# Performance work log

Measured on AMD Instinct MI355X. Metric: run time of the kernel, lower is better.

## Reference

```python
import jax, jax.numpy as jnp
import numpy as np

B, T, C, HEAD = 8, 2048, 1024, 64

def setup_inputs() -> dict:
    key = jax.random.key(0)
    kx, kq, kk, kv = jax.random.split(key, 4)
    bound = 1.0 / np.sqrt(C)  # torch Linear default init range
    x = jax.random.normal(kx, (B, T, C), dtype=jnp.float32)
    Wq = jax.random.uniform(kq, (C, HEAD), jnp.float32, -bound, bound)
    Wk = jax.random.uniform(kk, (C, HEAD), jnp.float32, -bound, bound)
    Wv = jax.random.uniform(kv, (C, HEAD), jnp.float32, -bound, bound)
    return {"x": x, "Wq": Wq, "Wk": Wk, "Wv": Wv}

def reference(x, Wq, Wk, Wv):
    Bn, Tn, Cn = x.shape
    q = jnp.einsum('btc,ch->bth', x, Wq)  # [B,T,H]
    k = jnp.einsum('btc,ch->bth', x, Wk)
    v = jnp.einsum('btc,ch->bth', x, Wv)
    # NOTE: original scales by C**-0.5 (input channels), not head_size**-0.5
    scale = Cn ** (-0.5)
    w = jnp.einsum('bqh,bkh->bqk', q, k) * scale  # [B,T,T]
    causal = jnp.tril(jnp.ones((Tn, Tn), dtype=bool))
    w = jnp.where(causal, w, -jnp.inf)
    wei = jax.nn.softmax(w, axis=-1)
    return jnp.einsum('bqk,bkh->bqh', wei, v)  # [B,T,H]
```

## Files before the change

kernel.cpp:

```cpp
#include <hip/hip_runtime.h>
#include <hip/hip_bf16.h>

#define B_ 8
#define T_ 2048
#define C_ 1024
#define H_ 64

typedef __bf16 bf16x8 __attribute__((ext_vector_type(8)));
typedef float f32x4 __attribute__((ext_vector_type(4)));

typedef __attribute__((address_space(3))) unsigned int lds_u32;
typedef const __attribute__((address_space(1))) unsigned int glb_u32;
__device__ __forceinline__ void gl_lds16(const void* gp, void* lp) {
  __builtin_amdgcn_global_load_lds((glb_u32*)gp, (lds_u32*)lp, 16, 0, 0);
}

__global__ __launch_bounds__(256) void prep_w_k(const float* __restrict__ Wq,
                                                const float* __restrict__ Wk,
                                                const float* __restrict__ Wv,
                                                __bf16* __restrict__ Wt2) {
  int idx = blockIdx.x * 256 + threadIdx.x;
  int m = idx >> 14;
  int rem = idx & 16383;
  int h = rem >> 8;
  int cb = (rem & 255) * 4;
  const float* W = (m == 0) ? Wq : ((m == 1) ? Wk : Wv);
  float sc = (m == 0) ? 0.03125f : 1.0f;
  const int col = m * 64 + h;
  const int t = cb >> 5;
  const int g = (cb >> 3) & 3;
  const int j = cb & 7;
  __bf16* dst = Wt2 + (((size_t)(t * 4 + g) * 192 + col) * 8 + j);
#pragma unroll
  for (int i = 0; i < 4; ++i) dst[i] = (__bf16)(W[(size_t)(cb + i) * H_ + h] * sc);
}

__global__ __launch_bounds__(256) void qkv_k(const float* __restrict__ x,
                                             const __bf16* __restrict__ Wt2,
                                             __bf16* __restrict__ q,
                                             __bf16* __restrict__ kk,
                                             __bf16* __restrict__ vt) {
  __shared__ __align__(16) char smem[65536];
  const int tid = threadIdx.x;
  const int lane = tid & 63;
  const int wc = tid >> 6;
  const int l15 = lane & 15;
  const int g = lane >> 4;
  const int row0 = blockIdx.x * 32;

  const int srow = tid >> 3;
  const int sch = (tid & 7) ^ (srow & 7);
  const char* agsrc = (const char*)(x + (size_t)(row0 + srow) * C_) + sch * 16;
  const int adst = tid * 16;
  const char* b2src = (const char*)Wt2 + tid * 16;

  f32x4 acc[2][3];
#pragma unroll
  for (int rt = 0; rt < 2; ++rt)
#pragma unroll
    for (int ctl = 0; ctl < 3; ++ctl) acc[rt][ctl] = (f32x4)0.0f;

  auto stage = [&](int t, int bufo) {
    gl_lds16(agsrc + ((size_t)t << 7), smem + bufo + adst);
    const char* bs = b2src + (size_t)t * 12288;
    gl_lds16(bs, smem + bufo + 4096 + tid * 16);
    gl_lds16(bs + 4096, smem + bufo + 8192 + tid * 16);
    gl_lds16(bs + 8192, smem + bufo + 12288 + tid * 16);
  };

  stage(0, 0);
  stage(1, 16384);
  stage(2, 32768);

  for (int t = 0; t < 32; ++t) {
    const int rem = 31 - t;
    if (rem >= 2) {
      asm volatile("s_waitcnt vmcnt(8)" ::: "memory");
    } else if (rem == 1) {
      asm volatile("s_waitcnt vmcnt(4)" ::: "memory");
    } else {
      asm volatile("s_waitcnt vmcnt(0)" ::: "memory");
    }
    __builtin_amdgcn_s_barrier();
    if (t + 3 < 32) stage(t + 3, ((t + 3) & 3) << 14);
    const int cur = (t & 3) << 14;
    bf16x8 af[2];
#pragma unroll
    for (int rt = 0; rt < 2; ++rt) {
      const int row = rt * 16 + l15;
      const char* ab = smem + cur + row * 128;
      f32x4 a0 = *(const f32x4*)(ab + ((((g << 1)) ^ (row & 7)) << 4));
      f32x4 a1 = *(const f32x4*)(ab + ((((g << 1) | 1) ^ (row & 7)) << 4));
#pragma unroll
      for (int j = 0; j < 4; ++j) {
        af[rt][j] = (__bf16)a0[j];
        af[rt][4 + j] = (__bf16)a1[j];
      }
    }
#pragma unroll
    for (int ctl = 0; ctl < 3; ++ctl) {
      const int col = wc * 48 + ctl * 16 + l15;
      bf16x8 bf = *(const bf16x8*)(smem + cur + 4096 + g * 3072 + col * 16);
      acc[0][ctl] = __builtin_amdgcn_mfma_f32_16x16x32_bf16(af[0], bf, acc[0][ctl], 0, 0, 0);
      acc[1][ctl] = __builtin_amdgcn_mfma_f32_16x16x32_bf16(af[1], bf, acc[1][ctl], 0, 0, 0);
    }
  }

#pragma unroll
  for (int rt = 0; rt < 2; ++rt)
#pragma unroll
    for (int ctl = 0; ctl < 3; ++ctl) {
      const int cb = wc * 48 + ctl * 16;
      const int m = cb >> 6;
      const int drow = row0 + rt * 16 + g * 4;
      if (m == 0) {
#pragma unroll
        for (int r = 0; r < 4; ++r)
          q[(size_t)(drow + r) * H_ + (cb & 63) + l15] = (__bf16)acc[rt][ctl][r];
      } else if (m == 1) {
#pragma unroll
        for (int r = 0; r < 4; ++r)
          kk[(size_t)(drow + r) * H_ + (cb & 63) + l15] = (__bf16)acc[rt][ctl][r];
      } else {
        const int vh = (cb - 128) + l15;
        const int t0 = rt * 16 + g * 4;
        union { ushort4 u; __bf16 h[4]; } pk;
#pragma unroll
        for (int r = 0; r < 4; ++r) pk.h[r] = (__bf16)acc[rt][ctl][r];
        int off = ((vh * 32 + t0) * 2) ^ ((vh & 7) << 4);
        *(ushort4*)(smem + off) = pk.u;
      }
    }
  __syncthreads();
  {
    const int h = tid >> 2;
    const int t8 = (tid & 3) * 8;
    const int sw = (h & 7) << 4;
    unsigned long long u0 = *(const unsigned long long*)(smem + (((h * 32 + t8) * 2) ^ sw));
    unsigned long long u1 = *(const unsigned long long*)(smem + (((h * 32 + t8 + 4) * 2) ^ sw));
    const int bb = blockIdx.x >> 6;
    const int tglob = (blockIdx.x & 63) * 32 + t8;
    unsigned long long* dst =
        (unsigned long long*)(vt + ((size_t)bb * 64 + h) * T_ + tglob);
    dst[0] = u0;
    dst[1] = u1;
  }
}

template <int SPLIT>
__global__ __launch_bounds__(256) void attn_k(const __bf16* __restrict__ q,
                                              const __bf16* __restrict__ k,
                                              const __bf16* __restrict__ vt,
                                              float* __restrict__ Opart,
                                              float2* __restrict__ ml) {
  __shared__ __align__(16) char smem[73728];
  const int bid = blockIdx.x;
  const int p = bid % SPLIT;
  const int qb = (bid / SPLIT) & 31;
  const int b = bid / (SPLIT * 32);
  const int tid = threadIdx.x;
  const int lane = tid & 63;
  const int w = tid >> 6;
  const int l15 = lane & 15;
  const int g = lane >> 4;
  const size_t qkbase = (size_t)b * T_ * H_;
  const int qr0 = qb * 64 + w * 16;

  const __bf16* qp = q + qkbase + (size_t)(qr0 + l15) * H_ + g * 8;
  bf16x8 aq0 = *(const bf16x8*)qp;
  bf16x8 aq1 = *(const bf16x8*)(qp + 32);
  asm volatile("s_waitcnt vmcnt(0)" ::: "memory");

  const int r0c = tid >> 3, x0c = (tid & 7) ^ (r0c & 7);
  const int r1c = (tid + 256) >> 3, x1c = (tid & 7) ^ (r1c & 7);
  const __bf16* ks0 = k + qkbase + (size_t)r0c * H_ + x0c * 8;
  const __bf16* ks1 = k + qkbase + (size_t)r1c * H_ + x1c * 8;
  const __bf16* vbase = vt + (size_t)b * 64 * T_;
  const __bf16* vs0 = vbase + (size_t)r0c * T_ + x0c * 8;
  const __bf16* vs1 = vbase + (size_t)r1c * T_ + x1c * 8;
  const int d0 = tid * 16, d1 = 4096 + tid * 16;

  auto stage = [&](int kvb, int bufo) {
    gl_lds16(ks0 + (size_t)kvb * H_, smem + bufo + d0);
    gl_lds16(ks1 + (size_t)kvb * H_, smem + bufo + d1);
    gl_lds16(vs0 + kvb, smem + bufo + 8192 + d0);
    gl_lds16(vs1 + kvb, smem + bufo + 8192 + d1);
  };

  f32x4 accO[4];
#pragma unroll
  for (int i = 0; i < 4; ++i) accO[i] = (f32x4)0.0f;
  float mrow[4] = {-1e30f, -1e30f, -1e30f, -1e30f};
  float lsum[4] = {0.f, 0.f, 0.f, 0.f};
  char* pb = smem + 65536 + w * 2048;

  const int len = (qb + SPLIT) / SPLIT;
  const int kb0 = p * len;
  int kbend = kb0 + len;
  if (kbend > qb + 1) kbend = qb + 1;
  const int n = kbend - kb0;

  if (n > 0) {
    stage(kb0 * 64, 0);
    if (n > 1) stage((kb0 + 1) * 64, 16384);
    if (n > 2) stage((kb0 + 2) * 64, 32768);
    for (int i = 0; i < n; ++i) {
      const int remn = n - 1 - i;
      if (remn >= 2) {
        asm volatile("s_waitcnt vmcnt(8)" ::: "memory");
      } else if (remn == 1) {
        asm volatile("s_waitcnt vmcnt(4)" ::: "memory");
      } else {
        asm volatile("s_waitcnt vmcnt(0)" ::: "memory");
      }
      __builtin_amdgcn_s_barrier();
      if (i + 3 < n) stage((kb0 + i + 3) * 64, ((i + 3) & 3) << 14);
      const int kb = kb0 + i;
      const int kvb = kb * 64;
      const char* kbuf = smem + ((i & 3) << 14);
      const char* vbuf = kbuf + 8192;
      f32x4 s[4];
#pragma unroll
      for (int ct = 0; ct < 4; ++ct) {
        const int row = ct * 16 + l15;
        bf16x8 b0 = *(const bf16x8*)(kbuf + row * 128 + ((g ^ (row & 7)) << 4));
        bf16x8 b1 = *(const bf16x8*)(kbuf + row * 128 + (((g + 4) ^ (row & 7)) << 4));
        f32x4 z = (f32x4)0.0f;
        z = __builtin_amdgcn_mfma_f32_16x16x32_bf16(aq0, b0, z, 0, 0, 0);
        z = __builtin_amdgcn_mfma_f32_16x16x32_bf16(aq1, b1, z, 0, 0, 0);
        s[ct] = z;
      }
      if (kb == qb) {
#pragma unroll
        for (int ct = 0; ct < 4; ++ct)
#pragma unroll
          for (int r = 0; r < 4; ++r)
            if (kvb + ct * 16 + l15 > qr0 + g * 4 + r) s[ct][r] = -1e30f;
      }
      float al[4];
#pragma unroll
      for (int r = 0; r < 4; ++r) {
        float v = fmaxf(fmaxf(s[0][r], s[1][r]), fmaxf(s[2][r], s[3][r]));
        v = fmaxf(v, __shfl_xor(v, 1, 64));
        v = fmaxf(v, __shfl_xor(v, 2, 64));
        v = fmaxf(v, __shfl_xor(v, 4, 64));
        v = fmaxf(v, __shfl_xor(v, 8, 64));
        float m2 = fmaxf(mrow[r], v);
        al[r] = __expf(mrow[r] - m2);
        mrow[r] = m2;
      }
#pragma unroll
      for (int ct = 0; ct < 4; ++ct)
#pragma unroll
        for (int r = 0; r < 4; ++r) s[ct][r] = __expf(s[ct][r] - mrow[r]);
#pragma unroll
      for (int r = 0; r < 4; ++r) {
        lsum[r] = lsum[r] * al[r] + (s[0][r] + s[1][r]) + (s[2][r] + s[3][r]);
#pragma unroll
        for (int hct = 0; hct < 4; ++hct) accO[hct][r] *= al[r];
      }
#pragma unroll
      for (int ct = 0; ct < 4; ++ct)
#pragma unroll
        for (int r = 0; r < 4; ++r) {
          int qrow = g * 4 + r;
          int off = ((qrow * 64 + ct * 16 + l15) * 2) ^ ((qrow & 7) << 4);
          *(__bf16*)(pb + off) = (__bf16)s[ct][r];
        }
#pragma unroll
      for (int ks = 0; ks < 2; ++ks) {
        int off = ((l15 * 64 + ks * 32 + g * 8) * 2) ^ ((l15 & 7) << 4);
        bf16x8 pa = *(const bf16x8*)(pb + off);
#pragma unroll
        for (int hct = 0; hct < 4; ++hct) {
          const int h = hct * 16 + l15;
          const int chunk = ks * 4 + g;
          bf16x8 bv = *(const bf16x8*)(vbuf + h * 128 + ((chunk ^ (h & 7)) << 4));
          accO[hct] = __builtin_amdgcn_mfma_f32_16x16x32_bf16(pa, bv, accO[hct], 0, 0, 0);
        }
      }
    }
  }
#pragma unroll
  for (int r = 0; r < 4; ++r) {
    float v = lsum[r];
    v += __shfl_xor(v, 1, 64);
    v += __shfl_xor(v, 2, 64);
    v += __shfl_xor(v, 4, 64);
    v += __shfl_xor(v, 8, 64);
    lsum[r] = v;
  }
  float* op = Opart + ((size_t)p * (B_ * T_) + (size_t)b * T_ + qr0) * H_;
#pragma unroll
  for (int hct = 0; hct < 4; ++hct)
#pragma unroll
    for (int r = 0; r < 4; ++r)
      op[(size_t)(g * 4 + r) * H_ + hct * 16 + l15] = accO[hct][r];
  if (l15 == 0) {
#pragma unroll
    for (int r = 0; r < 4; ++r)
      ml[(size_t)p * (B_ * T_) + (size_t)b * T_ + qr0 + g * 4 + r] =
          make_float2(mrow[r], lsum[r]);
  }
}

template <int SPLIT>
__global__ __launch_bounds__(256) void comb_k(const float* __restrict__ Opart,
                                              const float2* __restrict__ ml,
                                              float* __restrict__ out) {
  int gid = blockIdx.x * 256 + threadIdx.x;
  int row = gid >> 4;
  int h4 = (gid & 15) * 4;
  float m[SPLIT], l[SPLIT];
#pragma unroll
  for (int p = 0; p < SPLIT; ++p) {
    float2 t = ml[(size_t)p * (B_ * T_) + row];
    m[p] = t.x;
    l[p] = t.y;
  }
  float M = -1e30f;
#pragma unroll
  for (int p = 0; p < SPLIT; ++p) M = fmaxf(M, m[p]);
  float wp[SPLIT], wsum = 0.f;
#pragma unroll
  for (int p = 0; p < SPLIT; ++p) {
    wp[p] = __expf(m[p] - M);
    wsum += wp[p] * l[p];
  }
  float4 o = make_float4(0.f, 0.f, 0.f, 0.f);
#pragma unroll
  for (int p = 0; p < SPLIT; ++p) {
    float4 a = *(const float4*)(Opart + ((size_t)p * (B_ * T_) + row) * H_ + h4);
    o.x += wp[p] * a.x;
    o.y += wp[p] * a.y;
    o.z += wp[p] * a.z;
    o.w += wp[p] * a.w;
  }
  float inv = 1.0f / wsum;
  *(float4*)(out + (size_t)row * H_ + h4) =
      make_float4(o.x * inv, o.y * inv, o.z * inv, o.w * inv);
}

extern "C" void kernel_launch(void* const* d_in, const int* in_sizes, int n_in,
                              void* d_out, int out_size, void* d_ws, size_t ws_size,
                              hipStream_t stream) {
  const float* x  = (const float*)d_in[0];
  const float* Wq = (const float*)d_in[1];
  const float* Wk = (const float*)d_in[2];
  const float* Wv = (const float*)d_in[3];
  float* out = (float*)d_out;
  char* ws = (char*)d_ws;
  __bf16* Wt2  = (__bf16*)ws;
  __bf16* qb   = (__bf16*)(ws + 0x60000);
  __bf16* kb   = (__bf16*)(ws + 0x260000);
  __bf16* vtb  = (__bf16*)(ws + 0x460000);
  float*  Op   = (float*)(ws + 0x660000);
  float2* mlb  = (float2*)(ws + 0xE60000);

  hipLaunchKernelGGL(prep_w_k, dim3(192), dim3(256), 0, stream, Wq, Wk, Wv, Wt2);
  hipLaunchKernelGGL(qkv_k, dim3(512), dim3(256), 0, stream, x, Wt2, qb, kb, vtb);
  hipLaunchKernelGGL(attn_k<2>, dim3(8 * 32 * 2), dim3(256), 0, stream, qb, kb, vtb, Op, mlb);
  hipLaunchKernelGGL(comb_k<2>, dim3(1024), dim3(256), 0, stream, Op, mlb, out);
}
```

Measured before the change: 147.8 us.

## Enlarge QKV projection tile to 64 rows with 512 threads and deeper K-steps

The QKV projection kernel now uses 512-thread blocks that each compute 64 rows instead of 32. Two row-groups of waves share each staged weight tile, which halves how often the weight matrix is re-read per row. Each pipeline stage now covers 64 input channels instead of 32, using three 40KB LDS buffers (prefetch depth 2) in place of four 16KB buffers (depth 3). The cost is much higher LDS use per block, which lowers occupancy, and half as many blocks (256), which may leave some compute units idle.

```diff
diff --git a/kernel.cpp b/kernel.cpp
--- a/kernel.cpp
+++ b/kernel.cpp
@@ -35,24 +35,27 @@
   for (int i = 0; i < 4; ++i) dst[i] = (__bf16)(W[(size_t)(cb + i) * H_ + h] * sc);
 }
 
-__global__ __launch_bounds__(256) void qkv_k(const float* __restrict__ x,
+__global__ __launch_bounds__(512) void qkv_k(const float* __restrict__ x,
                                              const __bf16* __restrict__ Wt2,
                                              __bf16* __restrict__ q,
                                              __bf16* __restrict__ kk,
                                              __bf16* __restrict__ vt) {
-  __shared__ __align__(16) char smem[65536];
+  __shared__ __align__(16) char smem[122880];
   const int tid = threadIdx.x;
   const int lane = tid & 63;
-  const int wc = tid >> 6;
+  const int w = tid >> 6;
+  const int wr = w >> 2;
+  const int wc = w & 3;
   const int l15 = lane & 15;
   const int g = lane >> 4;
-  const int row0 = blockIdx.x * 32;
+  const int row0 = blockIdx.x * 64;
 
   const int srow = tid >> 3;
   const int sch = (tid & 7) ^ (srow & 7);
-  const char* agsrc = (const char*)(x + (size_t)(row0 + srow) * C_) + sch * 16;
+  const char* agsrc = (const char*)x + ((size_t)(row0 + srow) * C_ + 0) * 4 + sch * 16;
   const int adst = tid * 16;
   const char* b2src = (const char*)Wt2 + tid * 16;
+  const int bdst = 16384 + tid * 16;
 
   f32x4 acc[2][3];
 #pragma unroll
@@ -60,51 +63,56 @@
 #pragma unroll
     for (int ctl = 0; ctl < 3; ++ctl) acc[rt][ctl] = (f32x4)0.0f;
 
-  auto stage = [&](int t, int bufo) {
-    gl_lds16(agsrc + ((size_t)t << 7), smem + bufo + adst);
-    const char* bs = b2src + (size_t)t * 12288;
-    gl_lds16(bs, smem + bufo + 4096 + tid * 16);
-    gl_lds16(bs + 4096, smem + bufo + 8192 + tid * 16);
-    gl_lds16(bs + 8192, smem + bufo + 12288 + tid * 16);
+  auto stage = [&](int s, int bufo) {
+    const char* as = agsrc + (size_t)s * 256;
+    gl_lds16(as, smem + bufo + adst);
+    gl_lds16(as + 128, smem + bufo + 8192 + adst);
+    const char* bs = b2src + (size_t)s * 24576;
+    gl_lds16(bs, smem + bufo + bdst);
+    gl_lds16(bs + 8192, smem + bufo + 8192 + bdst);
+    gl_lds16(bs + 16384, smem + bufo + 16384 + bdst);
   };
 
   stage(0, 0);
-  stage(1, 16384);
-  stage(2, 32768);
-
-  for (int t = 0; t < 32; ++t) {
-    const int rem = 31 - t;
-    if (rem >= 2) {
-      asm volatile("s_waitcnt vmcnt(8)" ::: "memory");
-    } else if (rem == 1) {
-      asm volatile("s_waitcnt vmcnt(4)" ::: "memory");
+  stage(1, 40960);
+
+  for (int s = 0; s < 16; ++s) {
+    if (s < 15) {
+      asm volatile("s_waitcnt vmcnt(5)" ::: "memory");
     } else {
       asm volatile("s_waitcnt vmcnt(0)" ::: "memory");
     }
     __builtin_amdgcn_s_barrier();
-    if (t + 3 < 32) stage(t + 3, ((t + 3) & 3) << 14);
-    const int cur = (t & 3) << 14;
-    bf16x8 af[2];
-#pragma unroll
-    for (int rt = 0; rt < 2; ++rt) {
-      const int row = rt * 16 + l15;
-      const char* ab = smem + cur + row * 128;
-      f32x4 a0 = *(const f32x4*)(ab + ((((g << 1)) ^ (row & 7)) << 4));
-      f32x4 a1 = *(const f32x4*)(ab + ((((g << 1) | 1) ^ (row & 7)) << 4));
-#pragma unroll
-      for (int j = 0; j < 4; ++j) {
-        af[rt][j] = (__bf16)a0[j];
-        af[rt][4 + j] = (__bf16)a1[j];
+    if (s + 2 < 16) stage(s + 2, ((s + 2) % 3) * 40960);
+    const int bufo = (s % 3) * 40960;
+#pragma unroll
+    for (int kbr = 0; kbr < 2; ++kbr) {
+      const char* A = smem + bufo + kbr * 8192;
+      const char* Bq = smem + bufo + 16384 + kbr * 12288 + g * 3072;
+      bf16x8 af[2];
+#pragma unroll
+      for (int rt = 0; rt < 2; ++rt) {
+        const int row = wr * 32 + rt * 16 + l15;
+        const char* ab = A + row * 128;
+        f32x4 a0 = *(const f32x4*)(ab + ((((g << 1)) ^ (row & 7)) << 4));
+        f32x4 a1 = *(const f32x4*)(ab + ((((g << 1) | 1) ^ (row & 7)) << 4));
+#pragma unroll
+        for (int j = 0; j < 4; ++j) {
+          af[rt][j] = (__bf16)a0[j];
+          af[rt][4 + j] = (__bf16)a1[j];
+        }
+      }
+#pragma unroll
+      for (int ctl = 0; ctl < 3; ++ctl) {
+        const int col = wc * 48 + ctl * 16 + l15;
+        bf16x8 bf = *(const bf16x8*)(Bq + col * 16);
+        acc[0][ctl] = __builtin_amdgcn_mfma_f32_16x16x32_bf16(af[0], bf, acc[0][ctl], 0, 0, 0);
+        acc[1][ctl] = __builtin_amdgcn_mfma_f32_16x16x32_bf16(af[1], bf, acc[1][ctl], 0, 0, 0);
       }
     }
-#pragma unroll
-    for (int ctl = 0; ctl < 3; ++ctl) {
-      const int col = wc * 48 + ctl * 16 + l15;
-      bf16x8 bf = *(const bf16x8*)(smem + cur + 4096 + g * 3072 + col * 16);
-      acc[0][ctl] = __builtin_amdgcn_mfma_f32_16x16x32_bf16(af[0], bf, acc[0][ctl], 0, 0, 0);
-      acc[1][ctl] = __builtin_amdgcn_mfma_f32_16x16x32_bf16(af[1], bf, acc[1][ctl], 0, 0, 0);
-    }
-  }
+  }
+
+  __syncthreads();
 
 #pragma unroll
   for (int rt = 0; rt < 2; ++rt)
@@ -112,7 +120,7 @@
     for (int ctl = 0; ctl < 3; ++ctl) {
       const int cb = wc * 48 + ctl * 16;
       const int m = cb >> 6;
-      const int drow = row0 + rt * 16 + g * 4;
+      const int drow = row0 + wr * 32 + rt * 16 + g * 4;
       if (m == 0) {
 #pragma unroll
         for (int r = 0; r < 4; ++r)
@@ -123,27 +131,24 @@
           kk[(size_t)(drow + r) * H_ + (cb & 63) + l15] = (__bf16)acc[rt][ctl][r];
       } else {
         const int vh = (cb - 128) + l15;
-        const int t0 = rt * 16 + g * 4;
+        const int tl = wr * 32 + rt * 16 + g * 4;
         union { ushort4 u; __bf16 h[4]; } pk;
 #pragma unroll
         for (int r = 0; r < 4; ++r) pk.h[r] = (__bf16)acc[rt][ctl][r];
-        int off = ((vh * 32 + t0) * 2) ^ ((vh & 7) << 4);
+        int off = ((vh * 64 + tl) * 2) ^ ((vh & 7) << 4);
         *(ushort4*)(smem + off) = pk.u;
       }
     }
   __syncthreads();
   {
-    const int h = tid >> 2;
-    const int t8 = (tid & 3) * 8;
+    const int h = tid >> 3;
+    const int t8 = (tid & 7) * 8;
     const int sw = (h & 7) << 4;
-    unsigned long long u0 = *(const unsigned long long*)(smem + (((h * 32 + t8) * 2) ^ sw));
-    unsigned long long u1 = *(const unsigned long long*)(smem + (((h * 32 + t8 + 4) * 2) ^ sw));
-    const int bb = blockIdx.x >> 6;
-    const int tglob = (blockIdx.x & 63) * 32 + t8;
-    unsigned long long* dst =
-        (unsigned long long*)(vt + ((size_t)bb * 64 + h) * T_ + tglob);
-    dst[0] = u0;
-    dst[1] = u1;
+    union { uint4 u; char c[16]; } v;
+    v.u = *(const uint4*)(smem + (((h * 64 + t8) * 2) ^ sw));
+    const int bb = blockIdx.x >> 5;
+    const int tglob = (blockIdx.x & 31) * 64 + t8;
+    *(uint4*)(vt + ((size_t)bb * 64 + h) * T_ + tglob) = v.u;
   }
 }
 
@@ -358,7 +363,7 @@
   float2* mlb  = (float2*)(ws + 0xE60000);
 
   hipLaunchKernelGGL(prep_w_k, dim3(192), dim3(256), 0, stream, Wq, Wk, Wv, Wt2);
-  hipLaunchKernelGGL(qkv_k, dim3(512), dim3(256), 0, stream, x, Wt2, qb, kb, vtb);
+  hipLaunchKernelGGL(qkv_k, dim3(256), dim3(512), 0, stream, x, Wt2, qb, kb, vtb);
   hipLaunchKernelGGL(attn_k<2>, dim3(8 * 32 * 2), dim3(256), 0, stream, qb, kb, vtb, Op, mlb);
   hipLaunchKernelGGL(comb_k<2>, dim3(1024), dim3(256), 0, stream, Op, mlb, out);
 }
```

New measurement: 141.5 us. 1.04x faster.
